# Optimization experiments

Hardware: AMD Instinct MI355X
Metric: run time of the kernel (lower is better)

The kernel has to match this reference:

```python
import jax, jax.numpy as jnp
import numpy as np

TIME_SCALES = [1, 2, 4]
K = len(TIME_SCALES)      # 3 scales
N = 4                     # lcm(time_scales)
S = sum(TIME_SCALES)      # 7 slots
D_HEAD = 128              # d
D = S * D_HEAD            # 896
IO_DIM = 1024
RANK = 64
HIDDEN = 4 * D            # 3584
EPS = 1e-5


def _tables():
    active = np.empty((N, K), dtype=np.int64)
    perm = np.empty((N, K, N), dtype=np.int64)
    inv = np.empty((N, K, N), dtype=np.int64)
    ids = np.arange(N)
    for ph in range(N):
        off = 0
        for k, s in enumerate(TIME_SCALES):
            active[ph, k] = off + ph % s
            off += s
            j = ph % s
            alpha = N // s
            p = (ids + alpha * j) % N   # SHARED assignment
            perm[ph, k] = p
            ip = np.empty_like(p)
            ip[p] = ids
            inv[ph, k] = ip
    return active, perm, inv

ACTIVE, PERM, INV = _tables()


def _ln(x, scale, bias):
    mu = jnp.mean(x, axis=-1, keepdims=True)
    var = jnp.mean((x - mu) ** 2, axis=-1, keepdims=True)
    return (x - mu) * jax.lax.rsqrt(var + EPS) * scale + bias


def setup_inputs() -> dict:
    key = jax.random.key(0)
    ks = jax.random.split(key, 16)
    B, T = 8, 1024

    def w(k, shape, s=0.02):
        return jax.random.normal(k, shape, dtype=jnp.float32) * s

    return {
        "x": jax.random.normal(ks[0], (B, T, IO_DIM), dtype=jnp.float32),
        "enc_base_w": w(ks[1], (D, IO_DIM)),
        "enc_A_w": w(ks[2], (RANK, IO_DIM)),
        "enc_B": w(ks[3], (RANK, N, D)),
        "enc_beta": jnp.float32(0.01),
        "Wqkv": w(ks[4], (K, N, D_HEAD, 3 * D_HEAD)),
        "ln_attn_scale": jnp.ones((D_HEAD,), jnp.float32),
        "ln_attn_bias": jnp.zeros((D_HEAD,), jnp.float32),
        "ln_mixer_scale": jnp.ones((D,), jnp.float32),
        "ln_mixer_bias": jnp.zeros((D,), jnp.float32),
        "mixer_w1": w(ks[5], (HIDDEN, D)),
        "mixer_b1": jnp.zeros((HIDDEN,), jnp.float32),
        "mixer_w2": w(ks[6], (D, HIDDEN)),
        "mixer_b2": jnp.zeros((D,), jnp.float32),
        "dec_ln_scale": jnp.ones((N * D,), jnp.float32),
        "dec_ln_bias": jnp.zeros((N * D,), jnp.float32),
        "dec_down_w": w(ks[7], (RANK, N * D)),
        "dec_up_w": w(ks[8], (IO_DIM, RANK)),
        "phase": 1,
    }


def reference(x, enc_base_w, enc_A_w, enc_B, enc_beta, Wqkv,
              ln_attn_scale, ln_attn_bias, ln_mixer_scale, ln_mixer_bias,
              mixer_w1, mixer_b1, mixer_w2, mixer_b2,
              dec_ln_scale, dec_ln_bias, dec_down_w, dec_up_w, phase):
    B, T, _ = x.shape
    # ---- StreamLoRAEncoder: x [B,T,io] -> z0 [B,T,N,D]
    base = x @ enc_base_w.T                 # [B,T,D]
    h = x @ enc_A_w.T                       # [B,T,r]
    delta = jnp.einsum('btr,rnd->btnd', h, enc_B)
    z0 = base[:, :, None, :] + enc_beta * delta
    # ---- gather active slots for this phase (one slot per scale group)
    slots = ACTIVE[phase]                   # [K]
    z_slots = z0.reshape(B, T, N, S, D_HEAD)
    x_slot = z_slots[:, :, :, slots, :]     # [B,T,N,K,d]
    x_slot = _ln(x_slot, ln_attn_scale, ln_attn_bias)
    # ---- SHARED qkv projection (stream->head inverse perm, bmm, head->stream perm)
    x_in = x_slot.transpose(0, 1, 3, 2, 4)  # [B,T,K,N,d]
    kk = np.arange(K)[:, None]
    x_head = x_in[:, :, kk, INV[phase], :]  # [B,T,K,N,d]
    qkv = jnp.einsum('btknd,knde->btkne', x_head, Wqkv)  # [B,T,K,N,3d]
    qh, kh, vh = jnp.split(qkv, 3, axis=-1)
    p = PERM[phase]
    q = qh[:, :, kk, p, :].transpose(0, 3, 2, 1, 4).reshape(B, N * K, T, D_HEAD)
    k_ = kh[:, :, kk, p, :].transpose(0, 3, 2, 1, 4).reshape(B, N * K, T, D_HEAD)
    v = vh[:, :, kk, p, :].transpose(0, 3, 2, 1, 4).reshape(B, N * K, T, D_HEAD)
    # ---- causal attention over T per (stream, scale) head
    scores = jnp.einsum('bhtd,bhsd->bhts', q, k_) / np.float32(np.sqrt(D_HEAD))
    mask = jnp.tril(jnp.ones((T, T), dtype=bool))
    scores = jnp.where(mask, scores, jnp.float32(-1e9))
    attn = jax.nn.softmax(scores, axis=-1)
    out = jnp.einsum('bhts,bhsd->bhtd', attn, v)  # [B,N*K,T,d]
    # ---- scatter back to active slots (residual add)
    out5 = out.reshape(B, N, K, T, D_HEAD).transpose(0, 3, 1, 2, 4)  # [B,T,N,K,d]
    z1 = z_slots.at[:, :, :, slots, :].add(out5).reshape(B, T, N, D)
    # ---- mixer MLP (pre-LN residual)
    hm = _ln(z1, ln_mixer_scale, ln_mixer_bias)
    m = jax.nn.gelu(hm @ mixer_w1.T + mixer_b1, approximate=False) @ mixer_w2.T + mixer_b2
    z2 = z1 + m
    # ---- StreamLoRADecoder: concat streams, LN, rank-bottleneck projection
    cat = z2.reshape(B, T, N * D)
    y = _ln(cat, dec_ln_scale, dec_ln_bias) @ dec_down_w.T @ dec_up_w.T
    return y
```

## Files before the change

kernel.cpp:

```cpp
#include <hip/hip_runtime.h>
#include <hip/hip_bf16.h>
#include <math.h>


#define BT   8192
#define DH   128
#define DD   896
#define ND   3584
#define IO   1024
#define RK   64
#define HID  3584

typedef __attribute__((ext_vector_type(8))) short short8;
typedef __attribute__((ext_vector_type(4))) float f32x4;
typedef __hip_bfloat16 bf16;

#define DS_READ_B128(dst, p)                                                  \
    asm volatile("ds_read_b128 %0, %1"                                        \
                 : "=v"(dst)                                                  \
                 : "v"((const __attribute__((address_space(3))) bf16*)(p)))

__device__ __forceinline__ float gelu_f(float v)
{
    float u = v * 0.70710678118654752f;
    float a = fabsf(u);
    float t = __builtin_amdgcn_rcpf(1.0f + 0.3275911f * a);
    float p = t * (0.254829592f + t * (-0.284496736f + t * (1.421413741f +
              t * (-1.453152027f + t * 1.061405429f))));
    float er = 1.0f - p * __expf(-u * u);
    er = copysignf(er, u);
    return 0.5f * v * (1.0f + er);
}

template<int BM, int BN, int BK, int TM, int TN>
__global__ __launch_bounds__(256) void gemm_kernel(const float* __restrict__ A,
                                                   const float* __restrict__ B,
                                                   float* __restrict__ C,
                                                   int N, int Kd)
{
    constexpr int THREADS = (BM / TM) * (BN / TN);
    constexpr int LDA = BM + 4;
    constexpr int LDB = BN + 4;
    __shared__ float As[BK][LDA];
    __shared__ float Bs[BK][LDB];

    const int tid = threadIdx.x;
    constexpr int NX = BN / TN;
    const int tx = tid % NX;
    const int ty = tid / NX;
    const int row0 = blockIdx.y * BM;
    const int col0 = blockIdx.x * BN;

    float acc[TM][TN];
#pragma unroll
    for (int i = 0; i < TM; ++i)
#pragma unroll
        for (int j = 0; j < TN; ++j) acc[i][j] = 0.f;

    for (int k0 = 0; k0 < Kd; k0 += BK) {
        constexpr int AF4 = BM * BK / 4;
        for (int f = tid; f < AF4; f += THREADS) {
            int r  = f / (BK / 4);
            int c4 = (f % (BK / 4)) * 4;
            float4 v = *(const float4*)(A + (size_t)(row0 + r) * Kd + k0 + c4);
            As[c4 + 0][r] = v.x; As[c4 + 1][r] = v.y;
            As[c4 + 2][r] = v.z; As[c4 + 3][r] = v.w;
        }
        constexpr int BF4 = BN * BK / 4;
        for (int f = tid; f < BF4; f += THREADS) {
            int r  = f / (BK / 4);
            int c4 = (f % (BK / 4)) * 4;
            float4 v = *(const float4*)(B + (size_t)(col0 + r) * Kd + k0 + c4);
            Bs[c4 + 0][r] = v.x; Bs[c4 + 1][r] = v.y;
            Bs[c4 + 2][r] = v.z; Bs[c4 + 3][r] = v.w;
        }
        __syncthreads();

#pragma unroll
        for (int kk = 0; kk < BK; ++kk) {
            float a[TM], b[TN];
#pragma unroll
            for (int i = 0; i < TM; i += 4)
                *(float4*)&a[i] = *(const float4*)&As[kk][ty * TM + i];
#pragma unroll
            for (int j = 0; j < TN; j += 4)
                *(float4*)&b[j] = *(const float4*)&Bs[kk][tx * TN + j];
#pragma unroll
            for (int i = 0; i < TM; ++i)
#pragma unroll
                for (int j = 0; j < TN; ++j)
                    acc[i][j] = fmaf(a[i], b[j], acc[i][j]);
        }
        __syncthreads();
    }

    const int crow = row0 + ty * TM;
    const int ccol = col0 + tx * TN;
#pragma unroll
    for (int i = 0; i < TM; ++i) {
        float* cp = C + (size_t)(crow + i) * N + ccol;
#pragma unroll
        for (int j = 0; j < TN; ++j) cp[j] = acc[i][j];
    }
}

template<int BN, int EPI>
__global__ __launch_bounds__(512, 2) void gemm_bf16_256(
    const bf16* __restrict__ A,
    const bf16* __restrict__ B,
    float* __restrict__ Cf,
    bf16* __restrict__ Cb,
    int N, int Kd,
    const float* __restrict__ bias)
{
    constexpr int NR    = BN / 64;
    constexpr int WTN   = 16 * NR;
    constexpr int ASLOT = 256 * 32;
    constexpr int BSLOT = BN * 32;
    __shared__ bf16 As[4 * ASLOT];
    __shared__ bf16 Bs[4 * BSLOT];

    const int tid  = threadIdx.x;
    const int wave = tid >> 6;
    const int lane = tid & 63;
    const int wm = wave >> 2, wn = wave & 3;
    const int lr = lane & 15, lq = lane >> 4;

    const int gx  = gridDim.x;
    int fid = blockIdx.y * gx + blockIdx.x;
    const int cpx = (gx * gridDim.y) >> 3;
    fid = (fid & 7) * cpx + (fid >> 3);
    const int row0 = (fid / gx) * 256;
    const int col0 = (fid % gx) * BN;

    const int klen = Kd / (int)gridDim.z;
    const int kbeg = blockIdx.z * klen;

    const int sr  = lane >> 2;
    const int scs = (((lane & 3) ^ ((lane >> 3) & 3)) << 3);
    const bf16* Ag = A + (size_t)(row0 + sr) * Kd + kbeg + scs;
    const bf16* Bg = B + (size_t)(col0 + sr) * Kd + kbeg + scs;

    const int scox = (lq * 8) ^ (((lr >> 1) & 3) << 3);

    f32x4 acc[8][NR];
#pragma unroll
    for (int i = 0; i < 8; ++i)
#pragma unroll
        for (int j = 0; j < NR; ++j) acc[i][j] = (f32x4){0.f, 0.f, 0.f, 0.f};

    const int NH = klen >> 5;

    auto stage = [&](int h) {
        const int slot = h & 3;
#pragma unroll
        for (int i = 0; i < 2; ++i) {
            const int rg = (i * 8 + wave) * 16;
            __builtin_amdgcn_global_load_lds(
                (const __attribute__((address_space(1))) unsigned int*)
                    (Ag + (size_t)rg * Kd + h * 32),
                (__attribute__((address_space(3))) unsigned int*)
                    (As + slot * ASLOT + rg * 32),
                16, 0, 0);
        }
#pragma unroll
        for (int i = 0; i < BN / 128; ++i) {
            const int rg = (i * 8 + wave) * 16;
            __builtin_amdgcn_global_load_lds(
                (const __attribute__((address_space(1))) unsigned int*)
                    (Bg + (size_t)rg * Kd + h * 32),
                (__attribute__((address_space(3))) unsigned int*)
                    (Bs + slot * BSLOT + rg * 32),
                16, 0, 0);
        }
    };

    stage(0); stage(1); stage(2);

    for (int h = 0; h < NH; ++h) {
        if (h + 3 < NH) stage(h + 3);

        const int ahead = NH - 1 - h;
        if constexpr (BN == 256) {
            if (ahead >= 3)      asm volatile("s_waitcnt vmcnt(12)" ::: "memory");
            else if (ahead == 2) asm volatile("s_waitcnt vmcnt(8)"  ::: "memory");
            else if (ahead == 1) asm volatile("s_waitcnt vmcnt(4)"  ::: "memory");
            else                 asm volatile("s_waitcnt vmcnt(0)"  ::: "memory");
        } else {
            if (ahead >= 3)      asm volatile("s_waitcnt vmcnt(9)"  ::: "memory");
            else if (ahead == 2) asm volatile("s_waitcnt vmcnt(6)"  ::: "memory");
            else if (ahead == 1) asm volatile("s_waitcnt vmcnt(3)"  ::: "memory");
            else                 asm volatile("s_waitcnt vmcnt(0)"  ::: "memory");
        }
        __builtin_amdgcn_s_barrier();

        const bf16* Ab = As + (h & 3) * ASLOT;
        const bf16* Bb = Bs + (h & 3) * BSLOT;

        short8 bfr[NR], afr[8];
#pragma unroll
        for (int nt = 0; nt < NR; ++nt)
            DS_READ_B128(bfr[nt], Bb + (wn * WTN + nt * 16 + lr) * 32 + scox);
#pragma unroll
        for (int mt = 0; mt < 8; ++mt)
            DS_READ_B128(afr[mt], Ab + (wm * 128 + mt * 16 + lr) * 32 + scox);

        asm volatile("s_waitcnt lgkmcnt(4)" ::: "memory");
        __builtin_amdgcn_sched_barrier(0);

        __builtin_amdgcn_s_setprio(1);
#pragma unroll
        for (int mt = 0; mt < 4; ++mt)
#pragma unroll
            for (int nt = 0; nt < NR; ++nt)
                acc[mt][nt] = __builtin_amdgcn_mfma_f32_16x16x32_bf16(
                    afr[mt], bfr[nt], acc[mt][nt], 0, 0, 0);
        __builtin_amdgcn_s_setprio(0);

        asm volatile("s_waitcnt lgkmcnt(0)" ::: "memory");
        __builtin_amdgcn_sched_barrier(0);

        __builtin_amdgcn_s_setprio(1);
#pragma unroll
        for (int mt = 4; mt < 8; ++mt)
#pragma unroll
            for (int nt = 0; nt < NR; ++nt)
                acc[mt][nt] = __builtin_amdgcn_mfma_f32_16x16x32_bf16(
                    afr[mt], bfr[nt], acc[mt][nt], 0, 0, 0);
        __builtin_amdgcn_s_setprio(0);

        __builtin_amdgcn_s_barrier();
    }

#pragma unroll
    for (int mt = 0; mt < 8; ++mt) {
#pragma unroll
        for (int nt = 0; nt < NR; ++nt) {
            const int col = col0 + wn * WTN + nt * 16 + lr;
            const bool cok = (col < N);
            const float bcol = (EPI == 0 || EPI == 3 || !cok) ? 0.f : bias[col];
#pragma unroll
            for (int r = 0; r < 4; ++r) {
                const int row = row0 + wm * 128 + mt * 16 + lq * 4 + r;
                float v = acc[mt][nt][r] + bcol;
                if (EPI == 1) {
                    if (cok) Cb[(size_t)row * N + col] = __float2bfloat16(gelu_f(v));
                } else if (EPI == 2) {
                    if (cok) Cf[(size_t)row * N + col] += v;
                } else if (EPI == 3) {
                    if (cok) atomicAdd(Cf + (size_t)row * N + col, v);
                } else {
                    if (cok) Cf[(size_t)row * N + col] = v;
                }
            }
        }
    }
}

__global__ __launch_bounds__(256) void pack_enc_kernel(const float* __restrict__ baseW,
                                                       const float* __restrict__ Aw,
                                                       const float* __restrict__ Bv,
                                                       const float* __restrict__ betap,
                                                       bf16* __restrict__ outp)
{
    __shared__ float Ps[64][68];
    __shared__ float Qs[64][68];
    const int tid = threadIdx.x;
    const int e0 = blockIdx.y * 64;
    const int k0 = blockIdx.x * 64;

    for (int f = tid; f < 1024; f += 256) {
        int r = f >> 4, c4 = (f & 15) << 2;
        *(float4*)&Ps[r][c4] = *(const float4*)(Bv + (size_t)r * ND + e0 + c4);
        *(float4*)&Qs[r][c4] = *(const float4*)(Aw + (size_t)r * IO + k0 + c4);
    }
    __syncthreads();

    const int tx = tid & 15, ty = tid >> 4;
    float acc[4][4];
#pragma unroll
    for (int i = 0; i < 4; ++i)
#pragma unroll
        for (int j = 0; j < 4; ++j) acc[i][j] = 0.f;

#pragma unroll 8
    for (int r = 0; r < 64; ++r) {
        float a[4], b[4];
        *(float4*)a = *(const float4*)&Ps[r][ty * 4];
        *(float4*)b = *(const float4*)&Qs[r][tx * 4];
#pragma unroll
        for (int i = 0; i < 4; ++i)
#pragma unroll
            for (int j = 0; j < 4; ++j) acc[i][j] = fmaf(a[i], b[j], acc[i][j]);
    }

    const float beta = betap[0];
#pragma unroll
    for (int i = 0; i < 4; ++i) {
        const int e = e0 + ty * 4 + i;
        const int d = e % DD;
#pragma unroll
        for (int j = 0; j < 4; ++j) {
            const int k = k0 + tx * 4 + j;
            float v = baseW[(size_t)d * IO + k] + beta * acc[i][j];
            outp[(size_t)e * IO + k] = __float2bfloat16(v);
        }
    }
}

__global__ __launch_bounds__(256) void qkv_bf16_kernel(
    const bf16* __restrict__ xh,
    const bf16* __restrict__ Wt,
    bf16* __restrict__ Qg,
    bf16* __restrict__ Kg,
    bf16* __restrict__ Vtg,
    const int* __restrict__ phase_p,
    int go)
{
    __shared__ bf16 As[128 * 64];
    __shared__ bf16 Bs[128 * 64];

    const int ph  = phase_p[0] & 3;
    const int zbl = blockIdx.z;
    const int hh  = (go + zbl) % 12;
    const int n   = hh / 3;
    const int k   = hh % 3;
    const int m   = (k == 0) ? n
                  : (k == 1) ? ((n + 2 * (ph & 1)) & 3)
                             : ((n + (ph & 3)) & 3);
    const bf16* A  = xh + (size_t)zbl * (1024 * 128);
    const bf16* Bw = Wt + (size_t)(k * 4 + m) * (384 * 128);

    const int tid  = threadIdx.x;
    const int wave = tid >> 6;
    const int lane = tid & 63;
    const int wm = wave >> 1, wn = wave & 1;
    const int row0 = blockIdx.y * 128;
    const int col0 = blockIdx.x * 128;
    const int lr = lane & 15;
    const int lq = lane >> 4;
    const int srow = lane >> 3;
    const int scol = (lane & 7) * 8;

    f32x4 acc[4][4];
#pragma unroll
    for (int i = 0; i < 4; ++i)
#pragma unroll
        for (int j = 0; j < 4; ++j) acc[i][j] = (f32x4){0.f, 0.f, 0.f, 0.f};

#pragma unroll
    for (int k0 = 0; k0 < 128; k0 += 64) {
#pragma unroll
        for (int j = 0; j < 4; ++j) {
            const int rg = wave * 32 + j * 8;
            __builtin_amdgcn_global_load_lds(
                (const __attribute__((address_space(1))) unsigned int*)
                    (A + (size_t)(row0 + rg + srow) * 128 + k0 + scol),
                (__attribute__((address_space(3))) unsigned int*)(As + rg * 64),
                16, 0, 0);
        }
#pragma unroll
        for (int j = 0; j < 4; ++j) {
            const int rg = wave * 32 + j * 8;
            __builtin_amdgcn_global_load_lds(
                (const __attribute__((address_space(1))) unsigned int*)
                    (Bw + (size_t)(col0 + rg + srow) * 128 + k0 + scol),
                (__attribute__((address_space(3))) unsigned int*)(Bs + rg * 64),
                16, 0, 0);
        }
        __syncthreads();

#pragma unroll
        for (int s = 0; s < 64; s += 32) {
            short8 af[4], bf[4];
#pragma unroll
            for (int mt = 0; mt < 4; ++mt)
                af[mt] = *(const short8*)&As[(wm * 64 + mt * 16 + lr) * 64 + s + lq * 8];
#pragma unroll
            for (int nt = 0; nt < 4; ++nt)
                bf[nt] = *(const short8*)&Bs[(wn * 64 + nt * 16 + lr) * 64 + s + lq * 8];
#pragma unroll
            for (int mt = 0; mt < 4; ++mt)
#pragma unroll
                for (int nt = 0; nt < 4; ++nt)
                    acc[mt][nt] = __builtin_amdgcn_mfma_f32_16x16x32_bf16(
                        af[mt], bf[nt], acc[mt][nt], 0, 0, 0);
        }
        __syncthreads();
    }

    if (col0 < 256) {
        bf16* C = (col0 == 0 ? Qg : Kg) + (size_t)zbl * (1024 * 128);
#pragma unroll
        for (int mt = 0; mt < 4; ++mt)
#pragma unroll
            for (int nt = 0; nt < 4; ++nt) {
                const int col = wn * 64 + nt * 16 + lr;
#pragma unroll
                for (int r = 0; r < 4; ++r) {
                    const int row = row0 + wm * 64 + mt * 16 + lq * 4 + r;
                    C[(size_t)row * 128 + col] = __float2bfloat16(acc[mt][nt][r]);
                }
            }
    } else {
        bf16* Vt = Vtg + (size_t)zbl * (128 * 1024);
#pragma unroll
        for (int mt = 0; mt < 4; ++mt)
#pragma unroll
            for (int nt = 0; nt < 4; ++nt) {
                const int d = wn * 64 + nt * 16 + lr;
                const int rowb = row0 + wm * 64 + mt * 16 + lq * 4;
                union { bf16 h[4]; uint2 u; } pk;
#pragma unroll
                for (int r = 0; r < 4; ++r)
                    pk.h[r] = __float2bfloat16(acc[mt][nt][r]);
                *(uint2*)(Vt + (size_t)d * 1024 + rowb) = pk.u;
            }
    }
}

__global__ __launch_bounds__(512, 2) void flash_bf16_kernel(
    const bf16* __restrict__ Qg,
    const bf16* __restrict__ Kg,
    const bf16* __restrict__ Vtg,
    float* __restrict__ z,
    const int* __restrict__ phase_p,
    int go, int GQ)
{
    __shared__ bf16 Ks[2 * 64 * 128];
    __shared__ bf16 Vs[128 * 64];
    __shared__ bf16 Ps[128 * 64];

    const int ph   = phase_p[0] & 3;
    const int tid  = threadIdx.x;
    const int wave = tid >> 6;
    const int lane = tid & 63;
    const int lr = lane & 15;
    const int lq = lane >> 4;
    const int sr4 = lane >> 4, sc4 = (lane & 15) * 8;
    const int sr8 = lane >> 3, sc8 = (lane & 7) * 8;
    const int swz = (lr & 7) << 3;
    const float sc = 0.08838834764831845f;

    const int zbl = blockIdx.x % GQ;
    const int grp = blockIdx.x / GQ;
    const int zb  = go + zbl;
    const int b   = zb / 12;
    const int hh  = zb % 12;
    const int n   = hh / 3;
    const int ksl = hh % 3;
    const int slot = (ksl == 0) ? 0 : (ksl == 1 ? 1 + (ph & 1) : 3 + (ph & 3));

    const bf16* Qp = Qg  + (size_t)zbl * (1024 * 128);
    const bf16* Kp = Kg  + (size_t)zbl * (1024 * 128);
    const bf16* Vp = Vtg + (size_t)zbl * (128 * 1024);

    auto stageK = [&](int t) {
        const int j0 = t * 64;
        bf16* Kd = Ks + (t & 1) * (64 * 128);
#pragma unroll
        for (int j = 0; j < 2; ++j) {
            const int rg = wave * 8 + j * 4;
            const int krow = rg + sr4;
            const int kcol = sc4 ^ ((krow & 7) << 3);
            __builtin_amdgcn_global_load_lds(
                (const __attribute__((address_space(1))) unsigned int*)
                    (Kp + (size_t)(j0 + krow) * 128 + kcol),
                (__attribute__((address_space(3))) unsigned int*)(Kd + rg * 128),
                16, 0, 0);
        }
    };
    auto stageV = [&](int t) {
        const int j0 = t * 64;
#pragma unroll
        for (int j = 0; j < 2; ++j) {
            const int rg = wave * 16 + j * 8;
            const int vrow = rg + sr8;
            const int vcol = sc8 ^ ((vrow & 7) << 3);
            __builtin_amdgcn_global_load_lds(
                (const __attribute__((address_space(1))) unsigned int*)
                    (Vp + (size_t)vrow * 1024 + j0 + vcol),
                (__attribute__((address_space(3))) unsigned int*)(Vs + rg * 64),
                16, 0, 0);
        }
    };

    const int qa_t[5] = {7, 6, 5, 4, 3};
    const int qb_t[5] = {-1, 0, 1, 2, -1};

    for (int part = 0; part < 2; ++part) {
        const int qy8 = (part == 0) ? qa_t[grp] : qb_t[grp];
        if (qy8 < 0) break;
        const int q0  = qy8 * 128;
        const int NT  = qy8 * 2 + 2;

        short8 qreg[4];
#pragma unroll
        for (int s = 0; s < 4; ++s)
            qreg[s] = *(const short8*)(Qp + (size_t)(q0 + wave * 16 + lr) * 128
                                       + s * 32 + lq * 8);

        f32x4 accO[8];
        float m_i[4], l_i[4];
#pragma unroll
        for (int j = 0; j < 8; ++j) accO[j] = (f32x4){0.f, 0.f, 0.f, 0.f};
#pragma unroll
        for (int r = 0; r < 4; ++r) { m_i[r] = -1e30f; l_i[r] = 0.f; }

        stageK(0);

        for (int t = 0; t < NT; ++t) {
            const bool more = (t + 1 < NT);
            if (more) stageK(t + 1);
            stageV(t);
            if (more) asm volatile("s_waitcnt vmcnt(4)" ::: "memory");
            else      asm volatile("s_waitcnt vmcnt(2)" ::: "memory");
            __builtin_amdgcn_s_barrier();
            __builtin_amdgcn_sched_barrier(0);

            const bf16* Kbb = Ks + (t & 1) * (64 * 128);
            const int j0 = t * 64;
            const bool active = (j0 <= q0 + wave * 16 + 15);

            if (active) {
                f32x4 accS[4];
#pragma unroll
                for (int nt = 0; nt < 4; ++nt) accS[nt] = (f32x4){0.f, 0.f, 0.f, 0.f};
                short8 bk[2][4];
#pragma unroll
                for (int nt = 0; nt < 4; ++nt)
                    DS_READ_B128(bk[0][nt],
                                 Kbb + (nt * 16 + lr) * 128 + ((lq * 8) ^ swz));
#pragma unroll
                for (int s = 0; s < 4; ++s) {
                    if (s + 1 < 4) {
#pragma unroll
                        for (int nt = 0; nt < 4; ++nt)
                            DS_READ_B128(bk[(s + 1) & 1][nt],
                                         Kbb + (nt * 16 + lr) * 128
                                             + (((s + 1) * 32 + lq * 8) ^ swz));
                        asm volatile("s_waitcnt lgkmcnt(4)" ::: "memory");
                    } else {
                        asm volatile("s_waitcnt lgkmcnt(0)" ::: "memory");
                    }
                    __builtin_amdgcn_sched_barrier(0);
#pragma unroll
                    for (int nt = 0; nt < 4; ++nt)
                        accS[nt] = __builtin_amdgcn_mfma_f32_16x16x32_bf16(
                            qreg[s], bk[s & 1][nt], accS[nt], 0, 0, 0);
                }

                const bool need_mask = (j0 + 63 > q0 + wave * 16);
#pragma unroll
                for (int r = 0; r < 4; ++r) {
                    const int row = q0 + wave * 16 + lq * 4 + r;
                    float sv[4];
#pragma unroll
                    for (int nt = 0; nt < 4; ++nt) {
                        float v = accS[nt][r] * sc;
                        if (need_mask && (j0 + nt * 16 + lr > row)) v = -1e30f;
                        sv[nt] = v;
                    }
                    float mx = fmaxf(fmaxf(sv[0], sv[1]), fmaxf(sv[2], sv[3]));
#pragma unroll
                    for (int msk = 8; msk; msk >>= 1) mx = fmaxf(mx, __shfl_xor(mx, msk, 16));
                    float mnew = fmaxf(m_i[r], mx);
                    float al   = __expf(m_i[r] - mnew);
                    float rs = 0.f;
#pragma unroll
                    for (int nt = 0; nt < 4; ++nt) {
                        sv[nt] = __expf(sv[nt] - mnew);
                        rs += sv[nt];
                    }
#pragma unroll
                    for (int msk = 8; msk; msk >>= 1) rs += __shfl_xor(rs, msk, 16);
                    l_i[r] = l_i[r] * al + rs;
                    m_i[r] = mnew;
#pragma unroll
                    for (int d8 = 0; d8 < 8; ++d8) accO[d8][r] *= al;
                    const int prow = wave * 16 + lq * 4 + r;
                    const int pswz = (prow & 7) << 3;
#pragma unroll
                    for (int nt = 0; nt < 4; ++nt)
                        Ps[prow * 64 + ((nt * 16 + lr) ^ pswz)] = __float2bfloat16(sv[nt]);
                }
                asm volatile("" ::: "memory");
            }

            if (more) asm volatile("s_waitcnt vmcnt(2)" ::: "memory");
            else      asm volatile("s_waitcnt vmcnt(0)" ::: "memory");
            __builtin_amdgcn_s_barrier();
            __builtin_amdgcn_sched_barrier(0);

            if (active) {
                short8 ap[2], bv[2][8];
                DS_READ_B128(ap[0], Ps + (wave * 16 + lr) * 64 + ((lq * 8) ^ swz));
#pragma unroll
                for (int d8 = 0; d8 < 8; ++d8)
                    DS_READ_B128(bv[0][d8],
                                 Vs + (d8 * 16 + lr) * 64 + ((lq * 8) ^ swz));
#pragma unroll
                for (int kv = 0; kv < 2; ++kv) {
                    if (kv == 0) {
                        DS_READ_B128(ap[1],
                                     Ps + (wave * 16 + lr) * 64 + ((32 + lq * 8) ^ swz));
#pragma unroll
                        for (int d8 = 0; d8 < 8; ++d8)
                            DS_READ_B128(bv[1][d8],
                                         Vs + (d8 * 16 + lr) * 64 + ((32 + lq * 8) ^ swz));
                        asm volatile("s_waitcnt lgkmcnt(9)" ::: "memory");
                    } else {
                        asm volatile("s_waitcnt lgkmcnt(0)" ::: "memory");
                    }
                    __builtin_amdgcn_sched_barrier(0);
#pragma unroll
                    for (int d8 = 0; d8 < 8; ++d8)
                        accO[d8] = __builtin_amdgcn_mfma_f32_16x16x32_bf16(
                            ap[kv], bv[kv][d8], accO[d8], 0, 0, 0);
                }
            }

            __builtin_amdgcn_s_barrier();
        }

#pragma unroll
        for (int r = 0; r < 4; ++r) {
            const int t = q0 + wave * 16 + lq * 4 + r;
            const float inv = 1.0f / l_i[r];
            float* dst = z + (size_t)(b * 1024 + t) * ND + n * DD + slot * DH;
#pragma unroll
            for (int d8 = 0; d8 < 8; ++d8)
                dst[d8 * 16 + lr] += accO[d8][r] * inv;
        }
    }
}

__global__ __launch_bounds__(256) void cvt_bf16_kernel(const float* __restrict__ src,
                                                       bf16* __restrict__ dst,
                                                       int n4)
{
    int i = blockIdx.x * 256 + threadIdx.x;
    if (i < n4) {
        float4 v = ((const float4*)src)[i];
        bf16* d = dst + (size_t)i * 4;
        d[0] = __float2bfloat16(v.x);
        d[1] = __float2bfloat16(v.y);
        d[2] = __float2bfloat16(v.z);
        d[3] = __float2bfloat16(v.w);
    }
}

__global__ __launch_bounds__(256) void cvt_wqkv_kernel(const float* __restrict__ W,
                                                       bf16* __restrict__ Wt)
{
    int o = blockIdx.x * 256 + threadIdx.x;
    if (o < 12 * 384 * 128) {
        int i = o / 49152, rem = o % 49152;
        int e = rem / 128, d = rem % 128;
        Wt[o] = __float2bfloat16(W[(size_t)i * 49152 + d * 384 + e]);
    }
}

__global__ __launch_bounds__(256) void ln_attn_kernel(const float* __restrict__ z,
                                                      bf16* __restrict__ xh,
                                                      const float* __restrict__ scale,
                                                      const float* __restrict__ bias,
                                                      const int* __restrict__ phase_p,
                                                      int bt0)
{
    const int ph   = phase_p[0] & 3;
    const int lane = threadIdx.x & 63;
    const int row  = blockIdx.x * 4 + (threadIdx.x >> 6);
    const int k    = row % 3;
    const int n    = (row / 3) & 3;
    const int btl  = row / 12;
    const int slot = (k == 0) ? 0 : (k == 1 ? 1 + (ph & 1) : 3 + (ph & 3));
    const int bt   = bt0 + btl;

    const float* src = z + (size_t)bt * ND + n * DD + slot * DH + lane * 2;
    float2 v = *(const float2*)src;
    float s = v.x + v.y;
    float q = v.x * v.x + v.y * v.y;
#pragma unroll
    for (int m = 32; m; m >>= 1) { s += __shfl_xor(s, m); q += __shfl_xor(q, m); }
    float mu  = s * (1.0f / 128.0f);
    float var = q * (1.0f / 128.0f) - mu * mu;
    float r   = rsqrtf(var + 1e-5f);

    float2 sc2 = *(const float2*)(scale + lane * 2);
    float2 bi2 = *(const float2*)(bias + lane * 2);
    const int bl = btl >> 10, t = btl & 1023;
    union { bf16 h[2]; unsigned int u; } pk;
    pk.h[0] = __float2bfloat16((v.x - mu) * r * sc2.x + bi2.x);
    pk.h[1] = __float2bfloat16((v.y - mu) * r * sc2.y + bi2.y);
    *(unsigned int*)(xh + (size_t)((bl * 12 + n * 3 + k) * 1024 + t) * DH + lane * 2) = pk.u;
}

template<int W>
__global__ __launch_bounds__(256) void ln_row_bf16_kernel(const float* __restrict__ in,
                                                          bf16* __restrict__ outp,
                                                          const float* __restrict__ scale,
                                                          const float* __restrict__ bias)
{
    constexpr int NIT = (W + 255) / 256;
    const int row = blockIdx.x;
    const int tid = threadIdx.x;
    const float* rp = in + (size_t)row * W;

    float v[NIT];
    float s = 0.f, q = 0.f;
#pragma unroll
    for (int i = 0; i < NIT; ++i) {
        int idx = tid + i * 256;
        if (idx < W) { float t = rp[idx]; v[i] = t; s += t; q += t * t; }
        else v[i] = 0.f;
    }
#pragma unroll
    for (int m = 32; m; m >>= 1) { s += __shfl_xor(s, m); q += __shfl_xor(q, m); }
    __shared__ float ss[4], sq[4];
    if ((tid & 63) == 0) { ss[tid >> 6] = s; sq[tid >> 6] = q; }
    __syncthreads();
    s = ss[0] + ss[1] + ss[2] + ss[3];
    q = sq[0] + sq[1] + sq[2] + sq[3];
    float mu  = s * (1.0f / W);
    float var = q * (1.0f / W) - mu * mu;
    float r   = rsqrtf(var + 1e-5f);

    bf16* op = outp + (size_t)row * W;
#pragma unroll
    for (int i = 0; i < NIT; ++i) {
        int idx = tid + i * 256;
        if (idx < W)
            op[idx] = __float2bfloat16((v[i] - mu) * r * scale[idx] + bias[idx]);
    }
}

extern "C" void kernel_launch(void* const* d_in, const int* in_sizes, int n_in,
                              void* d_out, int out_size, void* d_ws, size_t ws_size,
                              hipStream_t stream)
{
    const float* x          = (const float*)d_in[0];
    const float* enc_base_w = (const float*)d_in[1];
    const float* enc_A_w    = (const float*)d_in[2];
    const float* enc_B      = (const float*)d_in[3];
    const float* enc_beta   = (const float*)d_in[4];
    const float* Wqkv       = (const float*)d_in[5];
    const float* ln_attn_s  = (const float*)d_in[6];
    const float* ln_attn_b  = (const float*)d_in[7];
    const float* ln_mix_s   = (const float*)d_in[8];
    const float* ln_mix_b   = (const float*)d_in[9];
    const float* w1         = (const float*)d_in[10];
    const float* b1         = (const float*)d_in[11];
    const float* w2         = (const float*)d_in[12];
    const float* b2         = (const float*)d_in[13];
    const float* dec_ln_s   = (const float*)d_in[14];
    const float* dec_ln_b   = (const float*)d_in[15];
    const float* dec_down   = (const float*)d_in[16];
    const float* dec_up     = (const float*)d_in[17];
    const int*   phase_p    = (const int*)d_in[18];
    float* out = (float*)d_out;

    float* ws = (float*)d_ws;
    float* z  = ws;
    float* R  = ws + (size_t)BT * ND;

    const int GQ = (ws_size >= 230000000UL) ? 96 : 48;
    const int CH = (ws_size >= 205000000UL) ? 8192 : 4096;

    bf16* xb   = (bf16*)R;
    bf16* Wenc = xb + (size_t)BT * IO;
    bf16* Wt   = (bf16*)R;
    bf16* xh_b = Wt + 12 * 384 * 128;
    bf16* Qb   = xh_b + (size_t)GQ * 1024 * 128;
    bf16* Kb   = Qb + (size_t)GQ * 1024 * 128;
    bf16* Vtg  = Kb + (size_t)GQ * 1024 * 128;
    bf16* w1b  = (bf16*)R;
    bf16* w2b  = w1b + (size_t)HID * DD;
    bf16* hm   = w2b + (size_t)DD * HID;
    bf16* gbuf = hm + (size_t)CH * DD;
    bf16*  zb  = (bf16*)R;
    bf16*  ddp = zb + (size_t)BT * ND;
    float* t1  = (float*)(ddp + 128 * ND);

    cvt_bf16_kernel<<<dim3(8192), 256, 0, stream>>>(x, xb, BT * IO / 4);
    pack_enc_kernel<<<dim3(16, 56), 256, 0, stream>>>(enc_base_w, enc_A_w, enc_B,
                                                      enc_beta, Wenc);
    gemm_bf16_256<256, 0><<<dim3(14, 32), 512, 0, stream>>>(xb, Wenc, z, nullptr,
                                                            ND, IO, nullptr);

    cvt_wqkv_kernel<<<dim3(2304), 256, 0, stream>>>(Wqkv, Wt);
    const int ngroups = 96 / GQ;
    for (int g = 0; g < ngroups; ++g) {
        ln_attn_kernel<<<dim3(GQ * 256), 256, 0, stream>>>(z, xh_b, ln_attn_s,
                                                           ln_attn_b, phase_p,
                                                           g * (GQ / 12) * 1024);
        qkv_bf16_kernel<<<dim3(3, 8, GQ), 256, 0, stream>>>(xh_b, Wt, Qb, Kb, Vtg,
                                                            phase_p, g * GQ);
        flash_bf16_kernel<<<dim3(GQ * 5), 512, 0, stream>>>(Qb, Kb, Vtg, z,
                                                            phase_p, g * GQ, GQ);
    }

    cvt_bf16_kernel<<<dim3(3136), 256, 0, stream>>>(w1, w1b, HID * DD / 4);
    cvt_bf16_kernel<<<dim3(3136), 256, 0, stream>>>(w2, w2b, DD * HID / 4);
    for (int c = 0; c < 32768 / CH; ++c) {
        float* zc = z + (size_t)c * CH * DD;
        ln_row_bf16_kernel<896><<<dim3(CH), 256, 0, stream>>>(zc, hm,
                                                              ln_mix_s, ln_mix_b);
        gemm_bf16_256<256, 1><<<dim3(14, CH / 256), 512, 0, stream>>>(
            hm, w1b, nullptr, gbuf, HID, DD, b1);
        gemm_bf16_256<128, 2><<<dim3(7, CH / 256), 512, 0, stream>>>(
            gbuf, w2b, zc, nullptr, DD, HID, b2);
    }

    ln_row_bf16_kernel<3584><<<dim3(8192), 256, 0, stream>>>(z, zb,
                                                             dec_ln_s, dec_ln_b);
    hipMemsetAsync(ddp + (size_t)64 * ND, 0, (size_t)64 * ND * sizeof(bf16),
                   stream);
    cvt_bf16_kernel<<<dim3(224), 256, 0, stream>>>(dec_down, ddp, 64 * ND / 4);
    hipMemsetAsync(t1, 0, (size_t)BT * RK * sizeof(float), stream);
    gemm_bf16_256<128, 3><<<dim3(1, 32, 8), 512, 0, stream>>>(zb, ddp, t1,
                                                              nullptr, RK, ND,
                                                              nullptr);
    gemm_kernel<128, 128, 16, 8, 8>
        <<<dim3(8, 64), 256, 0, stream>>>(t1, dec_up, out, IO, RK);
}
```

Before: 1.184 ms.

## Use atomic work queue for flash attention and double-buffer GEMM staging

```diff
diff --git a/kernel.cpp b/kernel.cpp
--- a/kernel.cpp
+++ b/kernel.cpp
@@ -117,8 +117,8 @@
     constexpr int WTN   = 16 * NR;
     constexpr int ASLOT = 256 * 32;
     constexpr int BSLOT = BN * 32;
-    __shared__ bf16 As[4 * ASLOT];
-    __shared__ bf16 Bs[4 * BSLOT];
+    __shared__ bf16 As[2 * ASLOT];
+    __shared__ bf16 Bs[2 * BSLOT];
 
     const int tid  = threadIdx.x;
     const int wave = tid >> 6;
@@ -152,7 +152,7 @@
     const int NH = klen >> 5;
 
     auto stage = [&](int h) {
-        const int slot = h & 3;
+        const int slot = h & 1;
 #pragma unroll
         for (int i = 0; i < 2; ++i) {
             const int rg = (i * 8 + wave) * 16;
@@ -175,27 +175,23 @@
         }
     };
 
-    stage(0); stage(1); stage(2);
+    stage(0);
 
     for (int h = 0; h < NH; ++h) {
-        if (h + 3 < NH) stage(h + 3);
-
-        const int ahead = NH - 1 - h;
+        const bool more = (h + 1 < NH);
+        if (more) stage(h + 1);
+
         if constexpr (BN == 256) {
-            if (ahead >= 3)      asm volatile("s_waitcnt vmcnt(12)" ::: "memory");
-            else if (ahead == 2) asm volatile("s_waitcnt vmcnt(8)"  ::: "memory");
-            else if (ahead == 1) asm volatile("s_waitcnt vmcnt(4)"  ::: "memory");
-            else                 asm volatile("s_waitcnt vmcnt(0)"  ::: "memory");
+            if (more) asm volatile("s_waitcnt vmcnt(4)" ::: "memory");
+            else      asm volatile("s_waitcnt vmcnt(0)" ::: "memory");
         } else {
-            if (ahead >= 3)      asm volatile("s_waitcnt vmcnt(9)"  ::: "memory");
-            else if (ahead == 2) asm volatile("s_waitcnt vmcnt(6)"  ::: "memory");
-            else if (ahead == 1) asm volatile("s_waitcnt vmcnt(3)"  ::: "memory");
-            else                 asm volatile("s_waitcnt vmcnt(0)"  ::: "memory");
+            if (more) asm volatile("s_waitcnt vmcnt(3)" ::: "memory");
+            else      asm volatile("s_waitcnt vmcnt(0)" ::: "memory");
         }
         __builtin_amdgcn_s_barrier();
 
-        const bf16* Ab = As + (h & 3) * ASLOT;
-        const bf16* Bb = Bs + (h & 3) * BSLOT;
+        const bf16* Ab = As + (h & 1) * ASLOT;
+        const bf16* Bb = Bs + (h & 1) * BSLOT;
 
         short8 bfr[NR], afr[8];
 #pragma unroll
@@ -425,11 +421,12 @@
     const bf16* __restrict__ Vtg,
     float* __restrict__ z,
     const int* __restrict__ phase_p,
-    int go, int GQ)
+    int go, int GQ, int* __restrict__ cnt)
 {
     __shared__ bf16 Ks[2 * 64 * 128];
     __shared__ bf16 Vs[128 * 64];
     __shared__ bf16 Ps[128 * 64];
+    __shared__ int sw;
 
     const int ph   = phase_p[0] & 3;
     const int tid  = threadIdx.x;
@@ -441,58 +438,60 @@
     const int sr8 = lane >> 3, sc8 = (lane & 7) * 8;
     const int swz = (lr & 7) << 3;
     const float sc = 0.08838834764831845f;
-
-    const int zbl = blockIdx.x % GQ;
-    const int grp = blockIdx.x / GQ;
-    const int zb  = go + zbl;
-    const int b   = zb / 12;
-    const int hh  = zb % 12;
-    const int n   = hh / 3;
-    const int ksl = hh % 3;
-    const int slot = (ksl == 0) ? 0 : (ksl == 1 ? 1 + (ph & 1) : 3 + (ph & 3));
-
-    const bf16* Qp = Qg  + (size_t)zbl * (1024 * 128);
-    const bf16* Kp = Kg  + (size_t)zbl * (1024 * 128);
-    const bf16* Vp = Vtg + (size_t)zbl * (128 * 1024);
-
-    auto stageK = [&](int t) {
-        const int j0 = t * 64;
-        bf16* Kd = Ks + (t & 1) * (64 * 128);
-#pragma unroll
-        for (int j = 0; j < 2; ++j) {
-            const int rg = wave * 8 + j * 4;
-            const int krow = rg + sr4;
-            const int kcol = sc4 ^ ((krow & 7) << 3);
-            __builtin_amdgcn_global_load_lds(
-                (const __attribute__((address_space(1))) unsigned int*)
-                    (Kp + (size_t)(j0 + krow) * 128 + kcol),
-                (__attribute__((address_space(3))) unsigned int*)(Kd + rg * 128),
-                16, 0, 0);
-        }
-    };
-    auto stageV = [&](int t) {
-        const int j0 = t * 64;
-#pragma unroll
-        for (int j = 0; j < 2; ++j) {
-            const int rg = wave * 16 + j * 8;
-            const int vrow = rg + sr8;
-            const int vcol = sc8 ^ ((vrow & 7) << 3);
-            __builtin_amdgcn_global_load_lds(
-                (const __attribute__((address_space(1))) unsigned int*)
-                    (Vp + (size_t)vrow * 1024 + j0 + vcol),
-                (__attribute__((address_space(3))) unsigned int*)(Vs + rg * 64),
-                16, 0, 0);
-        }
-    };
-
-    const int qa_t[5] = {7, 6, 5, 4, 3};
-    const int qb_t[5] = {-1, 0, 1, 2, -1};
-
-    for (int part = 0; part < 2; ++part) {
-        const int qy8 = (part == 0) ? qa_t[grp] : qb_t[grp];
-        if (qy8 < 0) break;
+    const int nitems = GQ * 8;
+
+    for (;;) {
+        __syncthreads();
+        if (tid == 0) sw = atomicAdd(cnt, 1);
+        __syncthreads();
+        const int w = sw;
+        if (w >= nitems) return;
+
+        const int wq  = w / GQ;
+        const int qy8 = 7 - wq;
+        const int zbl = w - wq * GQ;
+        const int zb  = go + zbl;
+        const int b   = zb / 12;
+        const int hh  = zb % 12;
+        const int n   = hh / 3;
+        const int ksl = hh % 3;
+        const int slot = (ksl == 0) ? 0 : (ksl == 1 ? 1 + (ph & 1) : 3 + (ph & 3));
         const int q0  = qy8 * 128;
         const int NT  = qy8 * 2 + 2;
+
+        const bf16* Qp = Qg  + (size_t)zbl * (1024 * 128);
+        const bf16* Kp = Kg  + (size_t)zbl * (1024 * 128);
+        const bf16* Vp = Vtg + (size_t)zbl * (128 * 1024);
+
+        auto stageK = [&](int t) {
+            const int j0 = t * 64;
+            bf16* Kd = Ks + (t & 1) * (64 * 128);
+#pragma unroll
+            for (int j = 0; j < 2; ++j) {
+                const int rg = wave * 8 + j * 4;
+                const int krow = rg + sr4;
+                const int kcol = sc4 ^ ((krow & 7) << 3);
+                __builtin_amdgcn_global_load_lds(
+                    (const __attribute__((address_space(1))) unsigned int*)
+                        (Kp + (size_t)(j0 + krow) * 128 + kcol),
+                    (__attribute__((address_space(3))) unsigned int*)(Kd + rg * 128),
+                    16, 0, 0);
+            }
+        };
+        auto stageV = [&](int t) {
+            const int j0 = t * 64;
+#pragma unroll
+            for (int j = 0; j < 2; ++j) {
+                const int rg = wave * 16 + j * 8;
+                const int vrow = rg + sr8;
+                const int vcol = sc8 ^ ((vrow & 7) << 3);
+                __builtin_amdgcn_global_load_lds(
+                    (const __attribute__((address_space(1))) unsigned int*)
+                        (Vp + (size_t)vrow * 1024 + j0 + vcol),
+                    (__attribute__((address_space(3))) unsigned int*)(Vs + rg * 64),
+                    16, 0, 0);
+            }
+        };
 
         short8 qreg[4];
 #pragma unroll
@@ -774,6 +773,7 @@
     bf16* Qb   = xh_b + (size_t)GQ * 1024 * 128;
     bf16* Kb   = Qb + (size_t)GQ * 1024 * 128;
     bf16* Vtg  = Kb + (size_t)GQ * 1024 * 128;
+    int*  cnt  = (int*)(Vtg + (size_t)GQ * 128 * 1024);
     bf16* w1b  = (bf16*)R;
     bf16* w2b  = w1b + (size_t)HID * DD;
     bf16* hm   = w2b + (size_t)DD * HID;
@@ -789,6 +789,7 @@
                                                             ND, IO, nullptr);
 
     cvt_wqkv_kernel<<<dim3(2304), 256, 0, stream>>>(Wqkv, Wt);
+    hipMemsetAsync(cnt, 0, 2 * sizeof(int), stream);
     const int ngroups = 96 / GQ;
     for (int g = 0; g < ngroups; ++g) {
         ln_attn_kernel<<<dim3(GQ * 256), 256, 0, stream>>>(z, xh_b, ln_attn_s,
@@ -796,8 +797,9 @@
                                                            g * (GQ / 12) * 1024);
         qkv_bf16_kernel<<<dim3(3, 8, GQ), 256, 0, stream>>>(xh_b, Wt, Qb, Kb, Vtg,
                                                             phase_p, g * GQ);
-        flash_bf16_kernel<<<dim3(GQ * 5), 512, 0, stream>>>(Qb, Kb, Vtg, z,
-                                                            phase_p, g * GQ, GQ);
+        flash_bf16_kernel<<<dim3(512), 512, 0, stream>>>(Qb, Kb, Vtg, z,
+                                                         phase_p, g * GQ, GQ,
+                                                         cnt + g);
     }
 
     cvt_bf16_kernel<<<dim3(3136), 256, 0, stream>>>(w1, w1b, HID * DD / 4);
```

Measured after the change: 1.157 ms. -2.2%, faster.
